# Kernel optimization log

Measured on AMD Instinct MI355X. Metric: run time of the kernel, lower is better.

## Reference

```python
import jax, jax.numpy as jnp
import numpy as np

N_GRAPHS, NODES_PER, DEG, D = 128, 1024, 32, 256
N = N_GRAPHS * NODES_PER          # 131072 nodes
E = N * DEG                       # 4194304 edges
RATIO = 0.8
K = int(np.ceil(RATIO * NODES_PER))  # 820 nodes kept per graph


def setup_inputs() -> dict:
    key = jax.random.key(0)
    k1, k2, k3, k4 = jax.random.split(key, 4)
    x = jax.random.normal(k1, (N, D), dtype=jnp.float32)
    # intra-graph random edges: endpoints within [0, NODES_PER) + graph offset
    src = jax.random.randint(k2, (E,), 0, NODES_PER)
    dst = jax.random.randint(k3, (E,), 0, NODES_PER)
    goff = (jnp.arange(E) // (NODES_PER * DEG)) * NODES_PER
    edge_index = jnp.stack([src + goff, dst + goff]).astype(jnp.int32)
    batch = jnp.repeat(jnp.arange(N_GRAPHS, dtype=jnp.int32), NODES_PER)
    W = jax.random.normal(k4, (D, 1), dtype=jnp.float32) / np.sqrt(D)
    b = jnp.zeros((1,), dtype=jnp.float32)
    return {"x": x, "edge_index": edge_index, "batch": batch, "W": W, "b": b}


def _gcn_score(x, edge_index, W, b):
    # GCNConv(in_channels, 1) with added self-loops and symmetric normalization
    n = x.shape[0]
    row, col = edge_index[0], edge_index[1]  # source, target
    # degree at target, init 1.0 accounts for self-loop
    deg = jnp.ones((n,), x.dtype).at[col].add(jnp.ones_like(col, dtype=x.dtype))
    dinv = jax.lax.rsqrt(deg)
    h = x @ W                                 # [n, 1]
    norm = dinv[row] * dinv[col]              # [E]
    agg = jnp.zeros_like(h).at[col].add(norm[:, None] * h[row])
    agg = agg + (dinv * dinv)[:, None] * h    # self-loop contribution deg^-1 * h_i
    return (agg + b).squeeze(-1)              # [n]


def reference(x, edge_index, batch, W, b):
    score = _gcn_score(x, edge_index, W, b)                     # [N]
    # per-graph top-k (graphs are contiguous, equal size)
    score_g = score.reshape(N_GRAPHS, NODES_PER)
    _, idx = jax.lax.top_k(score_g, K)                          # [G, K]
    perm = (idx + jnp.arange(N_GRAPHS)[:, None] * NODES_PER).reshape(-1)  # [G*K]
    x_new = x[perm] * jnp.tanh(score[perm])[:, None]            # [G*K, D]
    batch_new = batch[perm]
    # filter_adj: remap kept nodes to new ids, mask edges with dropped endpoints
    new_id = jnp.full((x.shape[0],), -1, dtype=perm.dtype).at[perm].set(
        jnp.arange(perm.shape[0], dtype=perm.dtype))
    r2 = new_id[edge_index[0]]
    c2 = new_id[edge_index[1]]
    edge_mask = (r2 >= 0) & (c2 >= 0)                           # [E] valid edges
    edge_index_new = jnp.where(edge_mask, jnp.stack([r2, c2]), -1)  # [2, E], -1 = dropped
    return x_new, edge_index_new, edge_mask, batch_new, perm
```

## Files before the change

kernel.cpp:

```cpp
#include <hip/hip_runtime.h>
#include <math.h>

constexpr int NG    = 128;
constexpr int NP    = 1024;
constexpr int D     = 256;
constexpr int NTOT  = NG * NP;
constexpr int EPG   = NP * 32;
constexpr int ET    = NTOT * 32;
constexpr int KK    = 820;
constexpr int NKEEP = NG * KK;

constexpr long long OUT_X     = 0;
constexpr long long OUT_EI0   = (long long)NKEEP * D;
constexpr long long OUT_EI1   = OUT_EI0 + ET;
constexpr long long OUT_MASK  = OUT_EI0 + 2LL * ET;
constexpr long long OUT_BATCH = OUT_MASK + ET;
constexpr long long OUT_PERM  = OUT_BATCH + NKEEP;

__global__ void node_init_kernel(const float* __restrict__ x,
                                 const float* __restrict__ W,
                                 float* __restrict__ h,
                                 int* __restrict__ new_id) {
    int row  = blockIdx.x * 4 + (threadIdx.x >> 6);
    int lane = threadIdx.x & 63;
    float4 a = ((const float4*)(x + (size_t)row * D))[lane];
    float4 w = ((const float4*)W)[lane];
    float s = a.x * w.x + a.y * w.y + a.z * w.z + a.w * w.w;
#pragma unroll
    for (int off = 32; off > 0; off >>= 1) s += __shfl_down(s, off, 64);
    if (lane == 0) {
        h[row]      = s;
        new_id[row] = -1;
    }
}

__global__ __launch_bounds__(1024) void graph_kernel(
        const int* __restrict__ rows, const int* __restrict__ cols,
        const float* __restrict__ h, const float* __restrict__ b,
        int* __restrict__ perm_i, int* __restrict__ new_id,
        float* __restrict__ factor,
        float* __restrict__ out_perm, float* __restrict__ out_batch) {
    __shared__ float h_l[NP];
    __shared__ float dv[NP];
    __shared__ float sc[NP];
    __shared__ int   si[NP];

    const int g = blockIdx.x;
    const int t = threadIdx.x;
    const int nbase = g * NP;

    h_l[t] = h[nbase + t];
    si[t]  = 1;
    __syncthreads();

    const int4* c4 = (const int4*)(cols + (size_t)g * EPG);
    const int4* r4 = (const int4*)(rows + (size_t)g * EPG);
#pragma unroll
    for (int i = t; i < EPG / 4; i += 1024) {
        int4 c = c4[i];
        atomicAdd(&si[c.x & (NP - 1)], 1);
        atomicAdd(&si[c.y & (NP - 1)], 1);
        atomicAdd(&si[c.z & (NP - 1)], 1);
        atomicAdd(&si[c.w & (NP - 1)], 1);
    }
    __syncthreads();

    {
        float di = 1.0f / sqrtf((float)si[t]);
        dv[t] = di;
        sc[t] = di * di * h_l[t] + b[0];
    }
    __syncthreads();
    si[t] = t;
    __syncthreads();

#pragma unroll
    for (int i = t; i < EPG / 4; i += 1024) {
        int4 c = c4[i];
        int4 r = r4[i];
        int lc, lr;
        lc = c.x & (NP - 1); lr = r.x & (NP - 1);
        atomicAdd(&sc[lc], dv[lr] * dv[lc] * h_l[lr]);
        lc = c.y & (NP - 1); lr = r.y & (NP - 1);
        atomicAdd(&sc[lc], dv[lr] * dv[lc] * h_l[lr]);
        lc = c.z & (NP - 1); lr = r.z & (NP - 1);
        atomicAdd(&sc[lc], dv[lr] * dv[lc] * h_l[lr]);
        lc = c.w & (NP - 1); lr = r.w & (NP - 1);
        atomicAdd(&sc[lc], dv[lr] * dv[lc] * h_l[lr]);
    }
    __syncthreads();

    for (int k = 2; k <= NP; k <<= 1) {
        for (int j = k >> 1; j > 0; j >>= 1) {
            int l = t ^ j;
            if (l > t) {
                float sv_t = sc[t], sv_l = sc[l];
                int   id_t = si[t], id_l = si[l];
                bool l_first = (sv_l > sv_t) || (sv_l == sv_t && id_l < id_t);
                if (l_first == ((t & k) == 0)) {
                    sc[t] = sv_l; sc[l] = sv_t;
                    si[t] = id_l; si[l] = id_t;
                }
            }
            __syncthreads();
        }
    }

    if (t < KK) {
        int node = nbase + si[t];
        int j    = g * KK + t;
        perm_i[j]    = node;
        new_id[node] = j;
        out_perm[j]  = (float)node;
        out_batch[j] = (float)g;
        factor[j]    = tanhf(sc[t]);
    }
}

__global__ void gather_kernel(const float* __restrict__ x,
                              const int* __restrict__ perm_i,
                              const float* __restrict__ factor,
                              float* __restrict__ out_x) {
    int j    = blockIdx.x * 4 + (threadIdx.x >> 6);
    int lane = threadIdx.x & 63;
    int node = perm_i[j];
    float t  = factor[j];
    float4 v = ((const float4*)(x + (size_t)node * D))[lane];
    float4 o = make_float4(v.x * t, v.y * t, v.z * t, v.w * t);
    ((float4*)(out_x + (size_t)j * D))[lane] = o;
}

__global__ void edge_kernel(const int* __restrict__ row, const int* __restrict__ col,
                            const int* __restrict__ new_id,
                            float* __restrict__ out_r, float* __restrict__ out_c,
                            float* __restrict__ out_m) {
    int t = blockIdx.x * blockDim.x + threadIdx.x;
    int4 r = ((const int4*)row)[t];
    int4 c = ((const int4*)col)[t];
    float4 fr, fc, fm;
    {
        int nr = new_id[r.x], nc = new_id[c.x];
        bool m = (nr >= 0) && (nc >= 0);
        fr.x = m ? (float)nr : -1.0f; fc.x = m ? (float)nc : -1.0f; fm.x = m ? 1.0f : 0.0f;
    }
    {
        int nr = new_id[r.y], nc = new_id[c.y];
        bool m = (nr >= 0) && (nc >= 0);
        fr.y = m ? (float)nr : -1.0f; fc.y = m ? (float)nc : -1.0f; fm.y = m ? 1.0f : 0.0f;
    }
    {
        int nr = new_id[r.z], nc = new_id[c.z];
        bool m = (nr >= 0) && (nc >= 0);
        fr.z = m ? (float)nr : -1.0f; fc.z = m ? (float)nc : -1.0f; fm.z = m ? 1.0f : 0.0f;
    }
    {
        int nr = new_id[r.w], nc = new_id[c.w];
        bool m = (nr >= 0) && (nc >= 0);
        fr.w = m ? (float)nr : -1.0f; fc.w = m ? (float)nc : -1.0f; fm.w = m ? 1.0f : 0.0f;
    }
    ((float4*)out_r)[t] = fr;
    ((float4*)out_c)[t] = fc;
    ((float4*)out_m)[t] = fm;
}

extern "C" void kernel_launch(void* const* d_in, const int* in_sizes, int n_in,
                              void* d_out, int out_size, void* d_ws, size_t ws_size,
                              hipStream_t stream) {
    const float* x  = (const float*)d_in[0];
    const int*   ei = (const int*)d_in[1];
    const float* W  = (const float*)d_in[3];
    const float* b  = (const float*)d_in[4];
    float* out = (float*)d_out;

    float* wsf    = (float*)d_ws;
    float* h      = wsf;
    int*   new_id = (int*)wsf + NTOT;
    int*   perm_i = (int*)wsf + 2 * NTOT;
    float* factor = wsf + 2 * NTOT + NKEEP;

    const int* rows = ei;
    const int* cols = ei + ET;

    hipLaunchKernelGGL(node_init_kernel, dim3(NTOT / 4), dim3(256), 0, stream,
                       x, W, h, new_id);
    hipLaunchKernelGGL(graph_kernel, dim3(NG), dim3(1024), 0, stream,
                       rows, cols, h, b, perm_i, new_id, factor,
                       out + OUT_PERM, out + OUT_BATCH);
    hipLaunchKernelGGL(gather_kernel, dim3(NKEEP / 4), dim3(256), 0, stream,
                       x, perm_i, factor, out + OUT_X);
    hipLaunchKernelGGL(edge_kernel, dim3(ET / 4 / 256), dim3(256), 0, stream,
                       rows, cols, new_id, out + OUT_EI0, out + OUT_EI1, out + OUT_MASK);
}
```

Before: 364.0 us.

## Pack score/index into sortable 64-bit keys and use wavefront shuffles in bitonic sort

The graph kernel now scatters di*h[row] into an accumulator and applies the target-side di once per node, instead of reading three shared arrays per edge. The bitonic top-k sort now packs each score, transformed to an order-preserving unsigned value, together with its index into one 64-bit key held in a register. Stages with stride below 64 exchange keys through wavefront shuffles and skip the block barriers; only larger strides go through shared memory. This is meant to cut shared-memory traffic and the number of __syncthreads in the sort, which dominates the single-block-per-graph kernel. Factoring out di changes the floating-point summation order slightly, which could flip ties near the top-k cutoff.

Result: faster. 355.9 us (-2.2%).

```diff
diff --git a/kernel.cpp b/kernel.cpp
--- a/kernel.cpp
+++ b/kernel.cpp
@@ -40,80 +40,82 @@
         int* __restrict__ perm_i, int* __restrict__ new_id,
         float* __restrict__ factor,
         float* __restrict__ out_perm, float* __restrict__ out_batch) {
-    __shared__ float h_l[NP];
-    __shared__ float dv[NP];
-    __shared__ float sc[NP];
-    __shared__ int   si[NP];
+    __shared__ float hl[NP];
+    __shared__ float uu[NP];
+    __shared__ float acc[NP];
+    __shared__ int   degc[NP];
+    __shared__ unsigned long long sk[NP];
 
     const int g = blockIdx.x;
     const int t = threadIdx.x;
     const int nbase = g * NP;
 
-    h_l[t] = h[nbase + t];
-    si[t]  = 1;
+    hl[t]   = h[nbase + t];
+    degc[t] = 1;
     __syncthreads();
 
     const int4* c4 = (const int4*)(cols + (size_t)g * EPG);
     const int4* r4 = (const int4*)(rows + (size_t)g * EPG);
+
 #pragma unroll
     for (int i = t; i < EPG / 4; i += 1024) {
         int4 c = c4[i];
-        atomicAdd(&si[c.x & (NP - 1)], 1);
-        atomicAdd(&si[c.y & (NP - 1)], 1);
-        atomicAdd(&si[c.z & (NP - 1)], 1);
-        atomicAdd(&si[c.w & (NP - 1)], 1);
+        atomicAdd(&degc[c.x & (NP - 1)], 1);
+        atomicAdd(&degc[c.y & (NP - 1)], 1);
+        atomicAdd(&degc[c.z & (NP - 1)], 1);
+        atomicAdd(&degc[c.w & (NP - 1)], 1);
     }
     __syncthreads();
 
-    {
-        float di = 1.0f / sqrtf((float)si[t]);
-        dv[t] = di;
-        sc[t] = di * di * h_l[t] + b[0];
-    }
-    __syncthreads();
-    si[t] = t;
+    float di = rsqrtf((float)degc[t]);
+    uu[t]  = di * hl[t];
+    acc[t] = 0.0f;
     __syncthreads();
 
 #pragma unroll
     for (int i = t; i < EPG / 4; i += 1024) {
         int4 c = c4[i];
         int4 r = r4[i];
-        int lc, lr;
-        lc = c.x & (NP - 1); lr = r.x & (NP - 1);
-        atomicAdd(&sc[lc], dv[lr] * dv[lc] * h_l[lr]);
-        lc = c.y & (NP - 1); lr = r.y & (NP - 1);
-        atomicAdd(&sc[lc], dv[lr] * dv[lc] * h_l[lr]);
-        lc = c.z & (NP - 1); lr = r.z & (NP - 1);
-        atomicAdd(&sc[lc], dv[lr] * dv[lc] * h_l[lr]);
-        lc = c.w & (NP - 1); lr = r.w & (NP - 1);
-        atomicAdd(&sc[lc], dv[lr] * dv[lc] * h_l[lr]);
+        atomicAdd(&acc[c.x & (NP - 1)], uu[r.x & (NP - 1)]);
+        atomicAdd(&acc[c.y & (NP - 1)], uu[r.y & (NP - 1)]);
+        atomicAdd(&acc[c.z & (NP - 1)], uu[r.z & (NP - 1)]);
+        atomicAdd(&acc[c.w & (NP - 1)], uu[r.w & (NP - 1)]);
     }
     __syncthreads();
 
+    float score = di * acc[t] + di * di * hl[t] + b[0];
+    hl[t] = score;
+
+    unsigned int fu = __float_as_uint(score);
+    unsigned int s  = (fu & 0x80000000u) ? ~fu : (fu | 0x80000000u);
+    unsigned long long key = ((unsigned long long)(~s) << 32) | (unsigned int)t;
+
     for (int k = 2; k <= NP; k <<= 1) {
         for (int j = k >> 1; j > 0; j >>= 1) {
-            int l = t ^ j;
-            if (l > t) {
-                float sv_t = sc[t], sv_l = sc[l];
-                int   id_t = si[t], id_l = si[l];
-                bool l_first = (sv_l > sv_t) || (sv_l == sv_t && id_l < id_t);
-                if (l_first == ((t & k) == 0)) {
-                    sc[t] = sv_l; sc[l] = sv_t;
-                    si[t] = id_l; si[l] = id_t;
-                }
+            unsigned long long other;
+            if (j < 64) {
+                other = __shfl_xor(key, j, 64);
+            } else {
+                sk[t] = key;
+                __syncthreads();
+                other = sk[t ^ j];
+                __syncthreads();
             }
-            __syncthreads();
+            bool take_min = (((t & k) == 0) == ((t & j) == 0));
+            bool omin = other < key;
+            key = (take_min == omin) ? other : key;
         }
     }
 
     if (t < KK) {
-        int node = nbase + si[t];
+        int idx  = (int)(key & 0xFFFFFFFFull);
+        int node = nbase + idx;
         int j    = g * KK + t;
         perm_i[j]    = node;
         new_id[node] = j;
         out_perm[j]  = (float)node;
         out_batch[j] = (float)g;
-        factor[j]    = tanhf(sc[t]);
+        factor[j]    = tanhf(hl[idx]);
     }
 }
 
```
